# Optimization experiments

Hardware: AMD Instinct MI355X
Metric: run time of the kernel (lower is better)

Reference implementation:

```python
import jax, jax.numpy as jnp
import numpy as np

NUM_TOKENS = 8192
TOKEN_DIM = 256
N = 65536
TOPK = 5
DECAY = 0.1      # cur_decay (set_decay_updates never called -> stays at init decay)
EPS = 1e-5
TEMP = 1.0


def setup_inputs() -> dict:
    key = jax.random.key(0)
    k1, k2 = jax.random.split(key)
    return {
        "inputs_flatten": jax.random.normal(k1, (N, TOKEN_DIM), dtype=jnp.float32),
        "embed": jax.random.normal(k2, (NUM_TOKENS, TOKEN_DIM), dtype=jnp.float32),
        "cluster_size": jnp.zeros((NUM_TOKENS,), dtype=jnp.float32),
        "cluster_sum": jnp.zeros((NUM_TOKENS,), dtype=jnp.float32),
        "embed_avg": jnp.zeros((NUM_TOKENS, TOKEN_DIM), dtype=jnp.float32),
    }


def reference(inputs_flatten, embed, cluster_size, cluster_sum, embed_avg):
    x = inputs_flatten                              # [N, D]
    # squared euclidean distances to codebook: [N, K]
    distances = (jnp.sum(x * x, axis=1, keepdims=True)
                 + jnp.sum(embed * embed, axis=1)
                 - 2.0 * (x @ embed.T))
    # top-k nearest codes (smallest distance)
    neg_topk, topk_idx = jax.lax.top_k(-distances, TOPK)   # [N, k]
    topk_dist = -neg_topk
    weights = jax.nn.softmax(-topk_dist / TEMP, axis=1)    # [N, k]
    # scatter soft weights into dense one-hot-ish encodings [N, K]
    rows = jnp.arange(x.shape[0])[:, None]
    encodings = jnp.zeros_like(distances).at[rows, topk_idx].set(weights)
    encoding_indices = jnp.argmax(encodings, axis=1)[:, None]   # [N, 1]

    # training-mode EMA codebook update (module default is training=True)
    encoding_sum = jnp.sum(encodings, axis=0)                   # [K]
    new_cluster_sum = cluster_sum + encoding_sum
    new_cluster_size = cluster_size * DECAY + encoding_sum * (1.0 - DECAY)
    embed_sum = encodings.T @ x                                 # [K, D]
    new_embed_avg = embed_avg * DECAY + embed_sum * (1.0 - DECAY)
    smoothed = (new_cluster_size + EPS) / (jnp.sum(new_cluster_size) + NUM_TOKENS * EPS)
    cs = smoothed * jnp.sum(new_cluster_size)
    new_embed = new_embed_avg / cs[:, None]                     # embed.data.copy_(...)

    quantize = encodings @ new_embed                            # [N, D]
    quantize = jax.lax.stop_gradient(quantize - x) + x          # straight-through
    return quantize, encoding_indices
```

## Files before the change

### kernel.cpp

```cpp
#include <hip/hip_runtime.h>
#include <hip/hip_bf16.h>
#include <math.h>
#include <limits.h>

#define NROWS 65536
#define DIM   256
#define NCODE 8192
#define NTOPK 5

typedef __attribute__((ext_vector_type(4))) float     f32x4;
typedef __attribute__((ext_vector_type(4))) int       i32x4;
typedef __attribute__((ext_vector_type(2))) unsigned  u32x2;

#define WS_ESWZ   0u
#define WS_CINIT  2097152u
#define WS_CAND   2129920u
#define WS_IDX5   4227072u
#define WS_W5     5537792u
#define WS_ENCSUM 6848512u
#define WS_CNT    6881280u
#define WS_OFFS   6914048u
#define WS_CURS   6946816u
#define WS_SFAC   6979584u
#define WS_ENTR   6979840u
#define WS_NEWEMB 9601280u

#define ENT_PER_BLK 64
#define NENT (NROWS * NTOPK)

__device__ __forceinline__ void gl_lds16(const void* g, void* l) {
  __builtin_amdgcn_global_load_lds(
      (const __attribute__((address_space(1))) unsigned int*)g,
      (__attribute__((address_space(3))) unsigned int*)l, 16, 0, 0);
}

__device__ __forceinline__ unsigned f2key(float f) {
  unsigned u = __float_as_uint(f);
  return (u & 0x80000000u) ? ~u : (u | 0x80000000u);
}
__device__ __forceinline__ float key2f(unsigned k) {
  unsigned u = (k & 0x80000000u) ? (k ^ 0x80000000u) : ~k;
  return __uint_as_float(u);
}

__global__ __launch_bounds__(256) void k_prep(const float* __restrict__ embed,
                                              signed char* __restrict__ eswz,
                                              int* __restrict__ cinit) {
  const int code = blockIdx.x;
  const int d = threadIdx.x;
  float v = embed[code * DIM + d];
  float qf = fminf(127.f, fmaxf(-127.f, rintf(16.f * v)));
  int q = (int)qf;
  __shared__ unsigned char rb[256];
  __shared__ int red[4];
  rb[d] = (unsigned char)(q & 255);
  int e2 = q * q;
  #pragma unroll
  for (int off = 32; off; off >>= 1) e2 += __shfl_down(e2, off);
  const int lane = d & 63, w = d >> 6;
  if (lane == 0) red[w] = e2;
  __syncthreads();
  if (d == 0) cinit[code] = -((red[0] + red[1] + red[2] + red[3]) >> 1);
  if (d < 64) {
    unsigned u = (unsigned)rb[4 * d] | ((unsigned)rb[4 * d + 1] << 8) |
                 ((unsigned)rb[4 * d + 2] << 16) | ((unsigned)rb[4 * d + 3] << 24);
    const int cs = (d >> 2) ^ (code & 15);
    ((unsigned*)(eswz + code * 256))[(cs << 2) | (d & 3)] = u;
  }
}


struct PList { int a, b, c, d; };

__device__ __forceinline__ void ladder(PList& P, int t) {
  int c0 = min(P.a, t); P.a = max(P.a, t);
  int c1 = min(P.b, c0); P.b = max(P.b, c0);
  int c2 = min(P.c, c1); P.c = max(P.c, c1);
  P.d = max(P.d, c2);
}

__device__ __forceinline__ void psel(PList& P, i32x4 acc, i32x4 en, int cb) {
  int p0 = ((acc[0] + en[0]) << 13) + cb;
  int p1 = ((acc[1] + en[1]) << 13) + cb + 1;
  int p2 = ((acc[2] + en[2]) << 13) + cb + 2;
  int p3 = ((acc[3] + en[3]) << 13) + cb + 3;
  int h1 = max(p0, p1);
  int h2 = max(p2, p3);
  int t1 = max(h1, h2);
  if (__any(t1 > P.d)) {
    int l1 = min(p0, p1), l2 = min(p2, p3);
    int t2 = max(min(h1, h2), max(l1, l2));
    ladder(P, t1);
    if (__any(t2 > P.d)) ladder(P, t2);
  }
}

__device__ __forceinline__ int pk4(f32x4 v) {
  int r = 0;
  #pragma unroll
  for (int j = 0; j < 4; ++j) {
    float q = fminf(127.f, fmaxf(-127.f, rintf(16.f * v[j])));
    r |= ((int)q & 255) << (8 * j);
  }
  return r;
}

__global__ __launch_bounds__(256, 2) void k_gemm(const float* __restrict__ x,
                                                 const signed char* __restrict__ eswz,
                                                 const int* __restrict__ cinit,
                                                 unsigned short* __restrict__ cand) {
  __shared__ signed char ebuf[3][8192];
  const int tid = threadIdx.x;
  const int lane = tid & 63, wave = tid >> 6;
  const int q = lane >> 4, ln = lane & 15;
  const int wrow0 = blockIdx.x * 128 + wave * 32;

  gl_lds16(eswz + tid * 16, &ebuf[0][tid * 16]);
  gl_lds16(eswz + 4096 + tid * 16, &ebuf[0][4096 + tid * 16]);

  i32x4 enc0 = *(const i32x4*)(cinit + q * 4);
  i32x4 enc1 = *(const i32x4*)(cinit + 16 + q * 4);

  i32x4 xf[2][4];
  #pragma unroll
  for (int t = 0; t < 2; ++t) {
    const float* xr = x + (unsigned)(wrow0 + t * 16 + ln) * DIM;
    #pragma unroll
    for (int s = 0; s < 4; ++s) {
      i32x4 dw;
      #pragma unroll
      for (int d = 0; d < 4; ++d)
        dw[d] = pk4(*(const f32x4*)(xr + s * 64 + q * 16 + d * 4));
      xf[t][s] = dw;
    }
  }

  PList P0 = {INT_MIN, INT_MIN, INT_MIN, INT_MIN};
  PList P1 = P0;

  int slot = 0;
  #pragma unroll 1
  for (int it = 0; it < 256; ++it) {
    const int nslot = (slot + 1 == 3) ? 0 : slot + 1;
    const int tl = (it < 255) ? it + 1 : 255;
    const signed char* src = eswz + (unsigned)tl * 8192;
    gl_lds16(src + tid * 16, &ebuf[nslot][tid * 16]);
    gl_lds16(src + 4096 + tid * 16, &ebuf[nslot][4096 + tid * 16]);
    i32x4 enn0 = *(const i32x4*)(cinit + tl * 32 + q * 4);
    i32x4 enn1 = *(const i32x4*)(cinit + tl * 32 + 16 + q * 4);

    asm volatile("s_waitcnt vmcnt(4)\n\ts_barrier" ::: "memory");

    const signed char* eb = ebuf[slot];
    i32x4 a00 = {0, 0, 0, 0}, a01 = a00, a10 = a00, a11 = a00;
    #pragma unroll
    for (int s = 0; s < 4; ++s) {
      const int chunk = (4 * s + q) ^ ln;
      i32x4 ea0 = *(const i32x4*)&eb[ln * 256 + chunk * 16];
      i32x4 ea1 = *(const i32x4*)&eb[4096 + ln * 256 + chunk * 16];
      a00 = __builtin_amdgcn_mfma_i32_16x16x64_i8(ea0, xf[0][s], a00, 0, 0, 0);
      a10 = __builtin_amdgcn_mfma_i32_16x16x64_i8(ea0, xf[1][s], a10, 0, 0, 0);
      a01 = __builtin_amdgcn_mfma_i32_16x16x64_i8(ea1, xf[0][s], a01, 0, 0, 0);
      a11 = __builtin_amdgcn_mfma_i32_16x16x64_i8(ea1, xf[1][s], a11, 0, 0, 0);
    }
    const int cb0 = it * 32 + q * 4, cb1 = cb0 + 16;
    psel(P0, a00, enc0, cb0);
    psel(P0, a01, enc1, cb1);
    psel(P1, a10, enc0, cb0);
    psel(P1, a11, enc1, cb1);

    enc0 = enn0; enc1 = enn1;
    slot = nslot;
  }

  {
    const int row0 = wrow0 + ln;
    u32x2 pk;
    pk[0] = ((unsigned)P0.a & 8191u) | (((unsigned)P0.b & 8191u) << 16);
    pk[1] = ((unsigned)P0.c & 8191u) | (((unsigned)P0.d & 8191u) << 16);
    *(u32x2*)&cand[row0 * 16 + q * 4] = pk;
    const int row1 = wrow0 + 16 + ln;
    pk[0] = ((unsigned)P1.a & 8191u) | (((unsigned)P1.b & 8191u) << 16);
    pk[1] = ((unsigned)P1.c & 8191u) | (((unsigned)P1.d & 8191u) << 16);
    *(u32x2*)&cand[row1 * 16 + q * 4] = pk;
  }
}

__global__ __launch_bounds__(256) void k_refine(const float* __restrict__ x,
                                                const float* __restrict__ embed,
                                                const unsigned short* __restrict__ cand,
                                                float* __restrict__ out_idx,
                                                int* __restrict__ idx5,
                                                float* __restrict__ w5,
                                                float* __restrict__ enc_sum,
                                                unsigned* __restrict__ cnt) {
  __shared__ float sh[4][16][66];
  const int wave = threadIdx.x >> 6, l = threadIdx.x & 63;
  const int row = blockIdx.x * 4 + wave;
  const float* xr = x + (unsigned)row * DIM;
  const f32x4 xv = *(const f32x4*)(xr + 4 * l);
  const float t0 = -2.f * xv[0], t1 = -2.f * xv[1];
  const float t2 = -2.f * xv[2], t3 = -2.f * xv[3];

  int cd[16];
  const unsigned* cp = (const unsigned*)(cand + row * 16);
  #pragma unroll
  for (int i = 0; i < 8; ++i) {
    unsigned v = cp[i];
    cd[2 * i] = (int)(v & 0xFFFFu);
    cd[2 * i + 1] = (int)(v >> 16);
  }

  #pragma unroll
  for (int ci = 0; ci < 16; ++ci) {
    const f32x4 e = *(const f32x4*)(embed + (unsigned)cd[ci] * DIM + 4 * l);
    float p = e[0] * (e[0] + t0);
    p = fmaf(e[1], e[1] + t1, p);
    p = fmaf(e[2], e[2] + t2, p);
    p = fmaf(e[3], e[3] + t3, p);
    sh[wave][ci][l] = p;
  }
  asm volatile("s_waitcnt lgkmcnt(0)" ::: "memory");

  const int c = l >> 2, sub = l & 3;
  const float* sp = &sh[wave][c][sub * 16];
  double s64 = 0.0;
  #pragma unroll
  for (int i = 0; i < 4; ++i) {
    f32x4 v = *(const f32x4*)(sp + i * 4);
    s64 += (double)v[0] + (double)v[1] + (double)v[2] + (double)v[3];
  }
  s64 += __shfl_xor(s64, 1);
  s64 += __shfl_xor(s64, 2);

  double sc = __shfl(s64, (l & 15) * 4);
  unsigned key = f2key((float)sc);
  const int myc = cd[l & 15];

  bool used = false;
  int codes[5]; float svals[5];
  #pragma unroll
  for (int j = 0; j < 5; ++j) {
    unsigned k = used ? 0xFFFFFFFFu : key;
    unsigned mm = k;
    #pragma unroll
    for (int off = 1; off < 16; off <<= 1) mm = min(mm, (unsigned)__shfl_xor((int)mm, off));
    int cc = (k == mm) ? myc : 0x7FFFFFFF;
    #pragma unroll
    for (int off = 1; off < 16; off <<= 1) cc = min(cc, __shfl_xor(cc, off));
    used = used || (myc == cc);
    codes[j] = cc;
    svals[j] = key2f(mm);
  }

  float ex[5], sum = 0.f;
  #pragma unroll
  for (int j = 0; j < 5; ++j) { ex[j] = expf(-(svals[j] - svals[0])); sum += ex[j]; }
  const float inv = 1.f / sum;

  if (l == 0) {
    out_idx[row] = (float)codes[0];
    #pragma unroll
    for (int j = 0; j < 5; ++j) {
      float w = ex[j] * inv;
      idx5[row * 5 + j] = codes[j];
      w5[row * 5 + j] = w;
      atomicAdd(&enc_sum[codes[j]], w);
      atomicAdd(&cnt[codes[j]], 1u);
    }
  }
}

__global__ __launch_bounds__(256) void k_scan(const unsigned* __restrict__ cnt,
                                              unsigned* __restrict__ offs,
                                              unsigned* __restrict__ cursor,
                                              const float* __restrict__ enc_sum,
                                              const float* __restrict__ cluster_size,
                                              float* __restrict__ sfac) {
  __shared__ unsigned part[256];
  __shared__ double sred[256];
  const int t = threadIdx.x;
  unsigned s = 0;
  for (int i = 0; i < 32; ++i) s += cnt[t * 32 + i];
  part[t] = s;
  double ds = 0.0;
  for (int i = t; i < NCODE; i += 256)
    ds += 0.1 * (double)cluster_size[i] + 0.9 * (double)enc_sum[i];
  sred[t] = ds;
  __syncthreads();
  if (t == 0) {
    unsigned run = 0;
    for (int i = 0; i < 256; ++i) { unsigned tmp = part[i]; part[i] = run; run += tmp; }
    double S = 0.0;
    for (int i = 0; i < 256; ++i) S += sred[i];
    sfac[0] = (float)(S / (S + (double)NCODE * 1e-5));
  }
  __syncthreads();
  unsigned off = part[t];
  for (int i = 0; i < 32; ++i) {
    unsigned c = cnt[t * 32 + i];
    offs[t * 32 + i] = off;
    cursor[t * 32 + i] = off;
    off += c;
  }
}

__global__ __launch_bounds__(256) void k_fill(const int* __restrict__ idx5,
                                              const float* __restrict__ w5,
                                              unsigned* __restrict__ cursor,
                                              uint2* __restrict__ entries) {
  const int i = blockIdx.x * 256 + threadIdx.x;
  if (i >= NENT) return;
  const unsigned c = (unsigned)idx5[i];
  const float w = w5[i];
  const unsigned row = (unsigned)i / 5u;
  const unsigned slot = atomicAdd(&cursor[c], 1u);
  entries[slot] = make_uint2((c << 16) | row, __float_as_uint(w));
}

__global__ __launch_bounds__(256) void k_accum2(const float* __restrict__ x,
                                                const uint2* __restrict__ entries,
                                                float* __restrict__ embsum) {
  __shared__ uint2 ent[ENT_PER_BLK];
  const int t = threadIdx.x;
  const unsigned base = blockIdx.x * ENT_PER_BLK;
  if (t < ENT_PER_BLK * 2)
    ((unsigned*)ent)[t] = ((const unsigned*)(entries + base))[t];
  __syncthreads();

  float acc = 0.f;
  unsigned cur = ent[0].x >> 16;
  #pragma unroll 8
  for (int i = 0; i < ENT_PER_BLK; ++i) {
    const uint2 e = ent[i];
    const unsigned code = e.x >> 16;
    const unsigned row = e.x & 0xFFFFu;
    const float w = __uint_as_float(e.y);
    if (code != cur) {
      atomicAdd(&embsum[cur * DIM + t], acc);
      acc = 0.f; cur = code;
    }
    acc = fmaf(w, x[row * DIM + t], acc);
  }
  atomicAdd(&embsum[cur * DIM + t], acc);
}

__global__ __launch_bounds__(256) void k_norm(const float* __restrict__ embed_avg,
                                              const float* __restrict__ cluster_size,
                                              const float* __restrict__ enc_sum,
                                              const float* __restrict__ sfac,
                                              float* __restrict__ embsum ) {
  const int k = blockIdx.x, d = threadIdx.x;
  const float ncs = 0.1f * cluster_size[k] + 0.9f * enc_sum[k];
  const float cs = (ncs + 1e-5f) * sfac[0];
  const unsigned o = (unsigned)k * DIM + d;
  embsum[o] = (0.1f * embed_avg[o] + 0.9f * embsum[o]) / cs;
}

__global__ __launch_bounds__(256) void k_quant(const int* __restrict__ idx5,
                                               const float* __restrict__ w5,
                                               const float* __restrict__ newemb,
                                               float* __restrict__ out) {
  const int d = threadIdx.x;
  const int rb = blockIdx.x * 16;
  #pragma unroll 2
  for (int r = 0; r < 16; ++r) {
    const int row = rb + r;
    float acc = 0.f;
    #pragma unroll
    for (int j = 0; j < 5; ++j)
      acc = fmaf(w5[row * 5 + j], newemb[(unsigned)idx5[row * 5 + j] * DIM + d], acc);
    out[(unsigned)row * DIM + d] = acc;
  }
}

extern "C" void kernel_launch(void* const* d_in, const int* in_sizes, int n_in,
                              void* d_out, int out_size, void* d_ws, size_t ws_size,
                              hipStream_t stream) {
  const float* x            = (const float*)d_in[0];
  const float* embed        = (const float*)d_in[1];
  const float* cluster_size = (const float*)d_in[2];
  const float* embed_avg    = (const float*)d_in[4];

  char* w = (char*)d_ws;
  signed char*    eswz   = (signed char*)(w + WS_ESWZ);
  int*            cinit  = (int*)(w + WS_CINIT);
  unsigned short* cand   = (unsigned short*)(w + WS_CAND);
  int*            idx5   = (int*)(w + WS_IDX5);
  float*          w5     = (float*)(w + WS_W5);
  float*          encsum = (float*)(w + WS_ENCSUM);
  unsigned*       cnt    = (unsigned*)(w + WS_CNT);
  unsigned*       offs   = (unsigned*)(w + WS_OFFS);
  unsigned*       curs   = (unsigned*)(w + WS_CURS);
  float*          sfac   = (float*)(w + WS_SFAC);
  uint2*          entr   = (uint2*)(w + WS_ENTR);
  float*          embsum = (float*)(w + WS_NEWEMB);

  float* out_q   = (float*)d_out;
  float* out_idx = out_q + (size_t)NROWS * DIM;

  hipMemsetAsync(w + WS_ENCSUM, 0, 65536, stream);
  hipMemsetAsync(w + WS_NEWEMB, 0, (size_t)NCODE * DIM * 4, stream);

  k_prep<<<NCODE, 256, 0, stream>>>(embed, eswz, cinit);
  k_gemm<<<NROWS / 128, 256, 0, stream>>>(x, eswz, cinit, cand);
  k_refine<<<NROWS / 4, 256, 0, stream>>>(x, embed, cand, out_idx, idx5, w5, encsum, cnt);
  k_scan<<<1, 256, 0, stream>>>(cnt, offs, curs, encsum, cluster_size, sfac);
  k_fill<<<(NENT + 255) / 256, 256, 0, stream>>>(idx5, w5, curs, entr);
  k_accum2<<<NENT / ENT_PER_BLK, 256, 0, stream>>>(x, entr, embsum);
  k_norm<<<NCODE, 256, 0, stream>>>(embed_avg, cluster_size, encsum, sfac, embsum);
  k_quant<<<NROWS / 16, 256, 0, stream>>>(idx5, w5, embsum, out_q);
}
```

Before: 466.3 us.

## Split codebook search across two blocks per row tile and refine 32 candidates

The int8 MFMA distance search is split so each row tile is handled by two blocks, each scanning half the codebook. That doubles the grid to improve occupancy and the latency hiding. Each half keeps its own top-4, so the exact fp32 refine kernel now rescoring 32 candidates instead of 16, which costs more embed gathers but raises candidate recall. The code index is folded into cinit ahead of time to save per-tile adds, s_setprio raises wave priority around the MFMA section, and the launch bounds target more resident blocks.

```diff
diff --git a/kernel.cpp b/kernel.cpp
--- a/kernel.cpp
+++ b/kernel.cpp
@@ -15,15 +15,15 @@
 #define WS_ESWZ   0u
 #define WS_CINIT  2097152u
 #define WS_CAND   2129920u
-#define WS_IDX5   4227072u
-#define WS_W5     5537792u
-#define WS_ENCSUM 6848512u
-#define WS_CNT    6881280u
-#define WS_OFFS   6914048u
-#define WS_CURS   6946816u
-#define WS_SFAC   6979584u
-#define WS_ENTR   6979840u
-#define WS_NEWEMB 9601280u
+#define WS_IDX5   6324224u
+#define WS_W5     7634944u
+#define WS_ENCSUM 8945664u
+#define WS_CNT    8978432u
+#define WS_OFFS   9011200u
+#define WS_CURS   9043968u
+#define WS_SFAC   9076736u
+#define WS_ENTR   9076992u
+#define WS_NEWEMB 11698432u
 
 #define ENT_PER_BLK 64
 #define NENT (NROWS * NTOPK)
@@ -60,7 +60,10 @@
   const int lane = d & 63, w = d >> 6;
   if (lane == 0) red[w] = e2;
   __syncthreads();
-  if (d == 0) cinit[code] = -((red[0] + red[1] + red[2] + red[3]) >> 1);
+  if (d == 0) {
+    int s = red[0] + red[1] + red[2] + red[3];
+    cinit[code] = -(s >> 1) * 8192 + code;
+  }
   if (d < 64) {
     unsigned u = (unsigned)rb[4 * d] | ((unsigned)rb[4 * d + 1] << 8) |
                  ((unsigned)rb[4 * d + 2] << 16) | ((unsigned)rb[4 * d + 3] << 24);
@@ -79,11 +82,11 @@
   P.d = max(P.d, c2);
 }
 
-__device__ __forceinline__ void psel(PList& P, i32x4 acc, i32x4 en, int cb) {
-  int p0 = ((acc[0] + en[0]) << 13) + cb;
-  int p1 = ((acc[1] + en[1]) << 13) + cb + 1;
-  int p2 = ((acc[2] + en[2]) << 13) + cb + 2;
-  int p3 = ((acc[3] + en[3]) << 13) + cb + 3;
+__device__ __forceinline__ void psel(PList& P, i32x4 acc, i32x4 en) {
+  int p0 = acc[0] * 8192 + en[0];
+  int p1 = acc[1] * 8192 + en[1];
+  int p2 = acc[2] * 8192 + en[2];
+  int p3 = acc[3] * 8192 + en[3];
   int h1 = max(p0, p1);
   int h2 = max(p2, p3);
   int t1 = max(h1, h2);
@@ -105,7 +108,7 @@
   return r;
 }
 
-__global__ __launch_bounds__(256, 2) void k_gemm(const float* __restrict__ x,
+__global__ __launch_bounds__(256, 4) void k_gemm(const float* __restrict__ x,
                                                  const signed char* __restrict__ eswz,
                                                  const int* __restrict__ cinit,
                                                  unsigned short* __restrict__ cand) {
@@ -113,13 +116,16 @@
   const int tid = threadIdx.x;
   const int lane = tid & 63, wave = tid >> 6;
   const int q = lane >> 4, ln = lane & 15;
-  const int wrow0 = blockIdx.x * 128 + wave * 32;
-
-  gl_lds16(eswz + tid * 16, &ebuf[0][tid * 16]);
-  gl_lds16(eswz + 4096 + tid * 16, &ebuf[0][4096 + tid * 16]);
-
-  i32x4 enc0 = *(const i32x4*)(cinit + q * 4);
-  i32x4 enc1 = *(const i32x4*)(cinit + 16 + q * 4);
+  const int half = blockIdx.x & 1, rb = blockIdx.x >> 1;
+  const int wrow0 = rb * 128 + wave * 32;
+  const signed char* esw_h = eswz + (unsigned)half * (4096u * 256u);
+  const int* cin_h = cinit + half * 4096;
+
+  gl_lds16(esw_h + tid * 16, &ebuf[0][tid * 16]);
+  gl_lds16(esw_h + 4096 + tid * 16, &ebuf[0][4096 + tid * 16]);
+
+  i32x4 enc0 = *(const i32x4*)(cin_h + q * 4);
+  i32x4 enc1 = *(const i32x4*)(cin_h + 16 + q * 4);
 
   i32x4 xf[2][4];
   #pragma unroll
@@ -140,19 +146,20 @@
 
   int slot = 0;
   #pragma unroll 1
-  for (int it = 0; it < 256; ++it) {
+  for (int it = 0; it < 128; ++it) {
     const int nslot = (slot + 1 == 3) ? 0 : slot + 1;
-    const int tl = (it < 255) ? it + 1 : 255;
-    const signed char* src = eswz + (unsigned)tl * 8192;
+    const int tl = (it < 127) ? it + 1 : 127;
+    const signed char* src = esw_h + (unsigned)tl * 8192;
     gl_lds16(src + tid * 16, &ebuf[nslot][tid * 16]);
     gl_lds16(src + 4096 + tid * 16, &ebuf[nslot][4096 + tid * 16]);
-    i32x4 enn0 = *(const i32x4*)(cinit + tl * 32 + q * 4);
-    i32x4 enn1 = *(const i32x4*)(cinit + tl * 32 + 16 + q * 4);
+    i32x4 enn0 = *(const i32x4*)(cin_h + tl * 32 + q * 4);
+    i32x4 enn1 = *(const i32x4*)(cin_h + tl * 32 + 16 + q * 4);
 
     asm volatile("s_waitcnt vmcnt(4)\n\ts_barrier" ::: "memory");
 
     const signed char* eb = ebuf[slot];
     i32x4 a00 = {0, 0, 0, 0}, a01 = a00, a10 = a00, a11 = a00;
+    __builtin_amdgcn_s_setprio(1);
     #pragma unroll
     for (int s = 0; s < 4; ++s) {
       const int chunk = (4 * s + q) ^ ln;
@@ -163,11 +170,11 @@
       a01 = __builtin_amdgcn_mfma_i32_16x16x64_i8(ea1, xf[0][s], a01, 0, 0, 0);
       a11 = __builtin_amdgcn_mfma_i32_16x16x64_i8(ea1, xf[1][s], a11, 0, 0, 0);
     }
-    const int cb0 = it * 32 + q * 4, cb1 = cb0 + 16;
-    psel(P0, a00, enc0, cb0);
-    psel(P0, a01, enc1, cb1);
-    psel(P1, a10, enc0, cb0);
-    psel(P1, a11, enc1, cb1);
+    __builtin_amdgcn_s_setprio(0);
+    psel(P0, a00, enc0);
+    psel(P0, a01, enc1);
+    psel(P1, a10, enc0);
+    psel(P1, a11, enc1);
 
     enc0 = enn0; enc1 = enn1;
     slot = nslot;
@@ -178,11 +185,11 @@
     u32x2 pk;
     pk[0] = ((unsigned)P0.a & 8191u) | (((unsigned)P0.b & 8191u) << 16);
     pk[1] = ((unsigned)P0.c & 8191u) | (((unsigned)P0.d & 8191u) << 16);
-    *(u32x2*)&cand[row0 * 16 + q * 4] = pk;
+    *(u32x2*)&cand[row0 * 32 + half * 16 + q * 4] = pk;
     const int row1 = wrow0 + 16 + ln;
     pk[0] = ((unsigned)P1.a & 8191u) | (((unsigned)P1.b & 8191u) << 16);
     pk[1] = ((unsigned)P1.c & 8191u) | (((unsigned)P1.d & 8191u) << 16);
-    *(u32x2*)&cand[row1 * 16 + q * 4] = pk;
+    *(u32x2*)&cand[row1 * 32 + half * 16 + q * 4] = pk;
   }
 }
 
@@ -194,7 +201,7 @@
                                                 float* __restrict__ w5,
                                                 float* __restrict__ enc_sum,
                                                 unsigned* __restrict__ cnt) {
-  __shared__ float sh[4][16][66];
+  __shared__ float sh[4][32][66];
   const int wave = threadIdx.x >> 6, l = threadIdx.x & 63;
   const int row = blockIdx.x * 4 + wave;
   const float* xr = x + (unsigned)row * DIM;
@@ -202,17 +209,17 @@
   const float t0 = -2.f * xv[0], t1 = -2.f * xv[1];
   const float t2 = -2.f * xv[2], t3 = -2.f * xv[3];
 
-  int cd[16];
-  const unsigned* cp = (const unsigned*)(cand + row * 16);
-  #pragma unroll
-  for (int i = 0; i < 8; ++i) {
+  int cd[32];
+  const unsigned* cp = (const unsigned*)(cand + row * 32);
+  #pragma unroll
+  for (int i = 0; i < 16; ++i) {
     unsigned v = cp[i];
     cd[2 * i] = (int)(v & 0xFFFFu);
     cd[2 * i + 1] = (int)(v >> 16);
   }
 
-  #pragma unroll
-  for (int ci = 0; ci < 16; ++ci) {
+  #pragma unroll 8
+  for (int ci = 0; ci < 32; ++ci) {
     const f32x4 e = *(const f32x4*)(embed + (unsigned)cd[ci] * DIM + 4 * l);
     float p = e[0] * (e[0] + t0);
     p = fmaf(e[1], e[1] + t1, p);
@@ -222,20 +229,19 @@
   }
   asm volatile("s_waitcnt lgkmcnt(0)" ::: "memory");
 
-  const int c = l >> 2, sub = l & 3;
-  const float* sp = &sh[wave][c][sub * 16];
+  const int c = l >> 1, sub = l & 1;
+  const float* sp = &sh[wave][c][sub * 32];
   double s64 = 0.0;
   #pragma unroll
-  for (int i = 0; i < 4; ++i) {
+  for (int i = 0; i < 8; ++i) {
     f32x4 v = *(const f32x4*)(sp + i * 4);
     s64 += (double)v[0] + (double)v[1] + (double)v[2] + (double)v[3];
   }
   s64 += __shfl_xor(s64, 1);
-  s64 += __shfl_xor(s64, 2);
-
-  double sc = __shfl(s64, (l & 15) * 4);
+
+  double sc = __shfl(s64, (l & 31) * 2);
   unsigned key = f2key((float)sc);
-  const int myc = cd[l & 15];
+  const int myc = cd[l & 31];
 
   bool used = false;
   int codes[5]; float svals[5];
@@ -244,10 +250,10 @@
     unsigned k = used ? 0xFFFFFFFFu : key;
     unsigned mm = k;
     #pragma unroll
-    for (int off = 1; off < 16; off <<= 1) mm = min(mm, (unsigned)__shfl_xor((int)mm, off));
+    for (int off = 1; off < 32; off <<= 1) mm = min(mm, (unsigned)__shfl_xor((int)mm, off));
     int cc = (k == mm) ? myc : 0x7FFFFFFF;
     #pragma unroll
-    for (int off = 1; off < 16; off <<= 1) cc = min(cc, __shfl_xor(cc, off));
+    for (int off = 1; off < 32; off <<= 1) cc = min(cc, __shfl_xor(cc, off));
     used = used || (myc == cc);
     codes[j] = cc;
     svals[j] = key2f(mm);
@@ -403,7 +409,7 @@
   hipMemsetAsync(w + WS_NEWEMB, 0, (size_t)NCODE * DIM * 4, stream);
 
   k_prep<<<NCODE, 256, 0, stream>>>(embed, eswz, cinit);
-  k_gemm<<<NROWS / 128, 256, 0, stream>>>(x, eswz, cinit, cand);
+  k_gemm<<<NROWS / 128 * 2, 256, 0, stream>>>(x, eswz, cinit, cand);
   k_refine<<<NROWS / 4, 256, 0, stream>>>(x, embed, cand, out_idx, idx5, w5, encsum, cnt);
   k_scan<<<1, 256, 0, stream>>>(cnt, offs, curs, encsum, cluster_size, sfac);
   k_fill<<<(NENT + 255) / 256, 256, 0, stream>>>(idx5, w5, curs, entr);
```

Measured after the change: 622.0 us. +33.4%, slower.
